# Optimization experiments

Hardware: AMD Instinct MI355X
Metric: run time of the kernel (lower is better)

Reference implementation:

```python
import jax, jax.numpy as jnp
import numpy as np

# FPN level layout for a 1024x1024 input image
LEVEL_HW = [(128, 128), (64, 64), (32, 32), (16, 16), (8, 8)]
STRIDES = [8, 16, 32, 64, 128]
IMG = 1024.0
NUM_CLASSES = 80
SCORE_THRESH = 0.2
NMS_THRESH = 0.6
TOPK = 1000
DETS = 100
BATCH = 8
TOTAL = sum(h * w for h, w in LEVEL_HW)  # 21824


def _make_anchors():
    rows = []
    for (h, w), s in zip(LEVEL_HW, STRIDES):
        xs = (np.arange(w, dtype=np.float32) + 0.5) * s
        ys = (np.arange(h, dtype=np.float32) + 0.5) * s
        xx, yy = np.meshgrid(xs, ys, indexing='ij')  # x-major, matches transpose(2,3) flatten
        pts = np.stack([xx.ravel(), yy.ravel(), xx.ravel(), yy.ravel()], axis=1)
        rows.append(pts)
    return np.concatenate(rows, axis=0).astype(np.float32)


def setup_inputs() -> dict:
    key = jax.random.key(0)
    k1, k2, k3 = jax.random.split(key, 3)
    cls_logits = jax.random.normal(k1, (BATCH, TOTAL, NUM_CLASSES), dtype=jnp.float32)
    bbox_regression = jax.random.uniform(k2, (BATCH, TOTAL, 4), dtype=jnp.float32) * 64.0
    bbox_ctrness = jax.random.normal(k3, (BATCH, TOTAL, 1), dtype=jnp.float32)
    anchors = jnp.asarray(_make_anchors())
    return {"cls_logits": cls_logits, "bbox_regression": bbox_regression,
            "bbox_ctrness": bbox_ctrness, "anchors": anchors}


def _iou_matrix(b):
    # b: [N,4] -> [N,N] pairwise IoU
    area = jnp.clip(b[:, 2] - b[:, 0], 0) * jnp.clip(b[:, 3] - b[:, 1], 0)
    lt = jnp.maximum(b[:, None, :2], b[None, :, :2])
    rb = jnp.minimum(b[:, None, 2:], b[None, :, 2:])
    wh = jnp.clip(rb - lt, 0)
    inter = wh[..., 0] * wh[..., 1]
    union = area[:, None] + area[None, :] - inter
    return inter / jnp.maximum(union, 1e-9)


def _postprocess_one(logits, reg, ctr, anchors):
    boxes_l, scores_l, labels_l = [], [], []
    off = 0
    for (h, w) in LEVEL_HW:
        n = h * w
        lg = logits[off:off + n]          # [n, C]
        rg = reg[off:off + n]             # [n, 4]
        ct = ctr[off:off + n, 0]          # [n]
        an = anchors[off:off + n]         # [n, 4]
        vals = lg.max(axis=-1)
        cls = jnp.argmax(lg, axis=-1)
        sc = jnp.sqrt(jax.nn.sigmoid(vals) * jax.nn.sigmoid(ct))
        # masked threshold + top-k  ==  filter-then-topk of the original
        masked = jnp.where(sc > SCORE_THRESH, sc, -1.0)
        k = min(TOPK, n)
        tv, ti = jax.lax.top_k(masked, k)
        a = an[ti]
        r = rg[ti]
        cx = (a[:, 0] + a[:, 2]) * 0.5
        cy = (a[:, 1] + a[:, 3]) * 0.5
        bx = jnp.stack([cx - r[:, 0], cy - r[:, 1], cx + r[:, 2], cy + r[:, 3]], axis=-1)
        bx = jnp.clip(bx, 0.0, IMG)       # clip_boxes_to_image
        boxes_l.append(bx)
        scores_l.append(tv)
        labels_l.append(cls[ti])
        off += n
    boxes = jnp.concatenate(boxes_l, axis=0)    # [N,4], N=3320
    scores = jnp.concatenate(scores_l, axis=0)  # [N]
    labels = jnp.concatenate(labels_l, axis=0)  # [N]
    N = boxes.shape[0]
    valid = scores > SCORE_THRESH
    order = jnp.argsort(-scores)
    boxes = boxes[order]
    scores = scores[order]
    labels = labels[order]
    valid = valid[order]
    # batched_nms: offset boxes per class so cross-class IoU is 0
    boff = boxes + (labels.astype(boxes.dtype) * (IMG + 1.0))[:, None]
    iou = _iou_matrix(boff)
    idx = jnp.arange(N)
    def body(i, active):
        sup = (iou[i] > NMS_THRESH) & (idx > i) & active[i]
        return active & ~sup
    active = jax.lax.fori_loop(0, N, body, valid)
    fsc = jnp.where(active, scores, -jnp.inf)
    tv, ti = jax.lax.top_k(fsc, DETS)
    m = tv > SCORE_THRESH
    out_boxes = jnp.where(m[:, None], boxes[ti], 0.0)
    out_scores = jnp.where(m, tv, 0.0)
    out_labels = jnp.where(m, labels[ti], -1)
    return out_boxes, out_scores, out_labels


def reference(cls_logits, bbox_regression, bbox_ctrness, anchors):
    fn = lambda l, r, c: _postprocess_one(l, r, c, anchors)
    boxes, scores, labels = jax.vmap(fn)(cls_logits, bbox_regression, bbox_ctrness)
    return boxes, scores, labels
```

## Files before the change

### kernel.cpp

```cpp
#include <hip/hip_runtime.h>
#include <stdint.h>

typedef unsigned long long u64;
typedef unsigned int u32;

#define BATCH   8
#define TOTAL   21824
#define NCLS    80
#define NDET    100
#define IMGSZ   1024.0f
#define STHR    0.2f
#define NMST    0.6f
#define NBUCK   2048
#define BMAX    2015
#define KGLOB   1000
#define NLOC    22

__device__ __forceinline__ float sigm(float x) { return 1.0f / (1.0f + expf(-x)); }

__device__ __forceinline__ u32 mapKm(float s) {
    u32 u = __float_as_uint(s);
    u32 m = u ^ ((u & 0x80000000u) ? 0xFFFFFFFFu : 0x80000000u);
    return ~m;
}
__device__ __forceinline__ u64 makeKey(float s, u32 idx) {
    return (((u64)mapKm(s)) << 32) | (u64)idx;
}

__device__ __forceinline__ int bucketOfV(float s) {
    int b = (int)(__fmul_rn(__fsub_rn(1.0f, s), 2520.0f));
    return b > BMAX ? BMAX : b;
}

__device__ __forceinline__ bool suppress(float4 a, float4 c) {
    float aa = __fmul_rn(fmaxf(__fsub_rn(a.z, a.x), 0.f), fmaxf(__fsub_rn(a.w, a.y), 0.f));
    float ac = __fmul_rn(fmaxf(__fsub_rn(c.z, c.x), 0.f), fmaxf(__fsub_rn(c.w, c.y), 0.f));
    float ltx = fmaxf(a.x, c.x), lty = fmaxf(a.y, c.y);
    float rbx = fminf(a.z, c.z), rby = fminf(a.w, c.w);
    float iw = fmaxf(__fsub_rn(rbx, ltx), 0.f), ih = fmaxf(__fsub_rn(rby, lty), 0.f);
    float inter = __fmul_rn(iw, ih);
    float uni = __fsub_rn(__fadd_rn(aa, ac), inter);
    float iou = __fdiv_rn(inter, fmaxf(uni, 1e-9f));
    return iou > NMST;
}

__global__ __launch_bounds__(256) void score_kernel(
        const float* __restrict__ logits, const float* __restrict__ ctr,
        float* __restrict__ mscore, int* __restrict__ mlabel) {
    const int b = blockIdx.y;
    const int tid = threadIdx.x;
    const int wave = tid >> 6, lane = tid & 63;
    const int g = lane >> 2, j = lane & 3;
    const int rowBase = blockIdx.x * 256 + wave * 64;
#pragma unroll
    for (int t = 0; t < 4; t++) {
        int r = rowBase + 16 * t + g;
        bool valid = r < TOTAL;
        float best = -1e30f; int bi = 0;
        if (valid) {
            const float* rowp = logits + ((size_t)b * TOTAL + r) * NCLS + j * 4;
#pragma unroll
            for (int u = 0; u < 5; u++) {
                float4 v = *(const float4*)(rowp + u * 16);
                int c0 = u * 16 + j * 4;
                if (v.x > best) { best = v.x; bi = c0; }
                if (v.y > best) { best = v.y; bi = c0 + 1; }
                if (v.z > best) { best = v.z; bi = c0 + 2; }
                if (v.w > best) { best = v.w; bi = c0 + 3; }
            }
        }
#pragma unroll
        for (int off = 1; off <= 2; off <<= 1) {
            float ob = __shfl_xor(best, off);
            int obi = __shfl_xor(bi, off);
            if (ob > best || (ob == best && obi < bi)) { best = ob; bi = obi; }
        }
        if (valid && j == 0) {
            float c = ctr[(size_t)b * TOTAL + r];
            float sc = sqrtf(sigm(best) * sigm(c));
            float msc = (sc > STHR) ? sc : -1.0f;
            mscore[(size_t)b * TOTAL + r] = msc;
            mlabel[(size_t)b * TOTAL + r] = bi;
        }
    }
}

__global__ __launch_bounds__(1024) void nms_kernel(
        const float* __restrict__ mscore, const int* __restrict__ mlabel,
        const float* __restrict__ anchors, const float* __restrict__ reg,
        float* __restrict__ out) {
    __shared__ u32 hist[NBUCK];
    __shared__ u64 skey[2048];
    __shared__ u32 waveSum[16], waveOff[16];
    __shared__ u32 sh_B, sh_m;
    __shared__ int s_count;
    __shared__ int accI[NDET];
    __shared__ float4 accB[NDET];
    __shared__ float4 accR[NDET];
    __shared__ int wIdx[64];
    __shared__ float4 wb[64], wraw[64];
    __shared__ u64 wsup[64];
    __shared__ u32 s_rej32[2];

    const int b = blockIdx.x, tid = threadIdx.x;
    const int wave = tid >> 6, lane = tid & 63;
    const float* ms = mscore + (size_t)b * TOTAL;

    hist[tid] = 0; hist[tid + 1024] = 0;
    if (tid == 0) { s_count = 0; sh_B = (u32)BMAX; }
    __syncthreads();

    float sv[NLOC];
    {
        int nl = 0;
        for (int i = tid; i < TOTAL; i += 1024) {
            float s0 = ms[i];
            sv[nl++] = s0;
            if (s0 > STHR) atomicAdd(&hist[bucketOfV(s0)], 1u);
        }
    }
    __syncthreads();

    u32 h0 = hist[2 * tid], h1 = hist[2 * tid + 1];
    u32 s = h0 + h1;
    u32 incl = s;
    for (int o = 1; o < 64; o <<= 1) {
        u32 t2 = (u32)__shfl_up((int)incl, o);
        if (lane >= o) incl += t2;
    }
    if (lane == 63) waveSum[wave] = incl;
    __syncthreads();
    if (tid == 0) {
        u32 acc = 0;
#pragma unroll
        for (int w = 0; w < 16; w++) { waveOff[w] = acc; acc += waveSum[w]; }
        sh_m = acc;
    }
    __syncthreads();
    const u32 E = waveOff[wave] + incl - s;
    if (E < KGLOB && KGLOB <= E + h0)            { sh_B = (u32)(2 * tid);     sh_m = E + h0; }
    else if (E + h0 < KGLOB && KGLOB <= E + h0 + h1) { sh_B = (u32)(2 * tid + 1); sh_m = E + h0 + h1; }
    hist[2 * tid] = E;
    hist[2 * tid + 1] = E + h0;
    __syncthreads();
    const int Bstar = (int)sh_B;

    {
        int nl = 0;
        for (int i = tid; i < TOTAL; i += 1024) {
            float s0 = sv[nl++];
            if (s0 > STHR) {
                int bk = bucketOfV(s0);
                if (bk <= Bstar) {
                    int pos = (int)atomicAdd(&hist[bk], 1u);
                    if (pos < 2048) skey[pos] = makeKey(s0, (u32)i);
                }
            }
        }
    }
    __syncthreads();

#pragma unroll
    for (int q = 0; q < 2; q++) {
        int bk = 2 * tid + q;
        u32 cnt = q ? h1 : h0;
        if (bk <= Bstar && cnt > 1) {
            int lo = (int)(q ? (E + h0) : E);
            int hi = lo + (int)cnt; if (hi > 2048) hi = 2048;
            for (int i2 = lo + 1; i2 < hi; i2++) {
                u64 key = skey[i2];
                int j2 = i2 - 1;
                while (j2 >= lo && skey[j2] > key) { skey[j2 + 1] = skey[j2]; j2--; }
                skey[j2 + 1] = key;
            }
        }
    }
    __syncthreads();
    int m = (int)sh_m; if (m > 2048) m = 2048;

    int count = 0, Ew = 0;
    while (true) {
        int take = m - Ew; if (take > 64) take = 64;
        if (take <= 0) break;

        if (tid < take) {
            int idx = (int)(skey[Ew + tid] & 0xFFFFFFFFu);
            float4 a = ((const float4*)anchors)[idx];
            float4 r = ((const float4*)reg)[(size_t)b * TOTAL + idx];
            float cx = (a.x + a.z) * 0.5f;
            float cy = (a.y + a.w) * 0.5f;
            float x1 = fminf(fmaxf(cx - r.x, 0.0f), IMGSZ);
            float y1 = fminf(fmaxf(cy - r.y, 0.0f), IMGSZ);
            float x2 = fminf(fmaxf(cx + r.z, 0.0f), IMGSZ);
            float y2 = fminf(fmaxf(cy + r.w, 0.0f), IMGSZ);
            float4 raw = make_float4(x1, y1, x2, y2);
            float off = (float)mlabel[(size_t)b * TOTAL + idx] * (IMGSZ + 1.0f);
            float4 ob = make_float4(__fadd_rn(x1, off), __fadd_rn(y1, off),
                                    __fadd_rn(x2, off), __fadd_rn(y2, off));
            wraw[tid] = raw; wb[tid] = ob; wIdx[tid] = idx;
        }
        if (tid < 2) s_rej32[tid] = 0;
        __syncthreads();

        {
            bool rej = false;
            if (lane < take) {
                for (int s2 = wave; s2 < count; s2 += 16) {
                    if (suppress(accB[s2], wb[lane])) { rej = true; break; }
                }
            }
            u64 mask = __ballot(rej);
            if (lane == 0 && mask) {
                u32 lo = (u32)mask, hi = (u32)(mask >> 32);
                if (lo) atomicOr(&s_rej32[0], lo);
                if (hi) atomicOr(&s_rej32[1], hi);
            }
        }
        for (int rr = wave; rr < take; rr += 16) {
            bool sp = false;
            if (lane < take && lane > rr) sp = suppress(wb[rr], wb[lane]);
            u64 mask = __ballot(sp);
            if (lane == 0) wsup[rr] = mask;
        }
        __syncthreads();

        if (wave == 0) {
            u64 supr = (lane < take) ? wsup[lane] : 0;
            u64 rejM = (u64)s_rej32[0] | ((u64)s_rej32[1] << 32);
            u64 aliveM = ((take >= 64) ? ~0ull : ((1ull << take) - 1ull)) & ~rejM;
            u64 accM = 0;
            for (int rr = 0; rr < take; rr++) {
                if ((aliveM >> rr) & 1) {
                    accM |= 1ull << rr;
                    u64 sr = __shfl(supr, rr);
                    aliveM &= ~sr;
                }
            }
            int na = __popcll(accM);
            int space = NDET - count;
            int takeA = na < space ? na : space;
            if (lane < take && ((accM >> lane) & 1)) {
                int pos = __popcll(accM & ((1ull << lane) - 1ull));
                if (pos < takeA) {
                    accI[count + pos] = wIdx[lane];
                    accB[count + pos] = wb[lane];
                    accR[count + pos] = wraw[lane];
                }
            }
            if (lane == 0) s_count = count + takeA;
        }
        __syncthreads();
        count = s_count;
        Ew += take;
        if (count >= NDET) break;
    }
    __syncthreads();

    for (int s2 = tid; s2 < NDET; s2 += 1024) {
        float4 bxv = make_float4(0.f, 0.f, 0.f, 0.f);
        float scv = 0.0f, lbv = -1.0f;
        if (s2 < count) {
            int idx = accI[s2];
            bxv = accR[s2];
            scv = ms[idx];
            lbv = (float)mlabel[(size_t)b * TOTAL + idx];
        }
        ((float4*)out)[b * NDET + s2] = bxv;
        out[BATCH * NDET * 4 + b * NDET + s2] = scv;
        out[BATCH * NDET * 4 + BATCH * NDET + b * NDET + s2] = lbv;
    }
}

extern "C" void kernel_launch(void* const* d_in, const int* in_sizes, int n_in,
                              void* d_out, int out_size, void* d_ws, size_t ws_size,
                              hipStream_t stream) {
    (void)in_sizes; (void)n_in; (void)out_size; (void)ws_size;
    const float* logits  = (const float*)d_in[0];
    const float* reg     = (const float*)d_in[1];
    const float* ctr     = (const float*)d_in[2];
    const float* anchors = (const float*)d_in[3];
    float* out = (float*)d_out;

    char* ws = (char*)d_ws;
    size_t off = 0;
    auto alloc = [&](size_t bytes) -> void* {
        off = (off + 255) & ~(size_t)255;
        void* p = ws + off;
        off += bytes;
        return p;
    };
    float* mscore = (float*)alloc((size_t)BATCH * TOTAL * 4);
    int*   mlabel = (int*)  alloc((size_t)BATCH * TOTAL * 4);

    score_kernel<<<dim3((TOTAL + 255) / 256, BATCH), 256, 0, stream>>>(logits, ctr, mscore, mlabel);
    nms_kernel<<<BATCH, 1024, 0, stream>>>(mscore, mlabel, anchors, reg, out);
}
```

Baseline: 145.0 us.

## Build score histogram in score kernel via global atomics instead of NMS kernel

```diff
diff --git a/kernel.cpp b/kernel.cpp
--- a/kernel.cpp
+++ b/kernel.cpp
@@ -44,9 +44,14 @@
     return iou > NMST;
 }
 
+__global__ __launch_bounds__(256) void zero_hist(u32* __restrict__ g) {
+    ((uint4*)g)[blockIdx.x * 256 + threadIdx.x] = make_uint4(0u, 0u, 0u, 0u);
+}
+
 __global__ __launch_bounds__(256) void score_kernel(
         const float* __restrict__ logits, const float* __restrict__ ctr,
-        float* __restrict__ mscore, int* __restrict__ mlabel) {
+        float* __restrict__ mscore, int* __restrict__ mlabel,
+        u32* __restrict__ ghist) {
     const int b = blockIdx.y;
     const int tid = threadIdx.x;
     const int wave = tid >> 6, lane = tid & 63;
@@ -78,9 +83,10 @@
         if (valid && j == 0) {
             float c = ctr[(size_t)b * TOTAL + r];
             float sc = sqrtf(sigm(best) * sigm(c));
-            float msc = (sc > STHR) ? sc : -1.0f;
-            mscore[(size_t)b * TOTAL + r] = msc;
+            bool pass = sc > STHR;
+            mscore[(size_t)b * TOTAL + r] = pass ? sc : -1.0f;
             mlabel[(size_t)b * TOTAL + r] = bi;
+            if (pass) atomicAdd(&ghist[(size_t)b * NBUCK + bucketOfV(sc)], 1u);
         }
     }
 }
@@ -88,8 +94,8 @@
 __global__ __launch_bounds__(1024) void nms_kernel(
         const float* __restrict__ mscore, const int* __restrict__ mlabel,
         const float* __restrict__ anchors, const float* __restrict__ reg,
-        float* __restrict__ out) {
-    __shared__ u32 hist[NBUCK];
+        const u32* __restrict__ ghist, float* __restrict__ out) {
+    __shared__ u32 cur[NBUCK];
     __shared__ u64 skey[2048];
     __shared__ u32 waveSum[16], waveOff[16];
     __shared__ u32 sh_B, sh_m;
@@ -106,22 +112,16 @@
     const int wave = tid >> 6, lane = tid & 63;
     const float* ms = mscore + (size_t)b * TOTAL;
 
-    hist[tid] = 0; hist[tid + 1024] = 0;
-    if (tid == 0) { s_count = 0; sh_B = (u32)BMAX; }
-    __syncthreads();
+    uint2 hv = ((const uint2*)(ghist + (size_t)b * NBUCK))[tid];
 
     float sv[NLOC];
-    {
-        int nl = 0;
-        for (int i = tid; i < TOTAL; i += 1024) {
-            float s0 = ms[i];
-            sv[nl++] = s0;
-            if (s0 > STHR) atomicAdd(&hist[bucketOfV(s0)], 1u);
-        }
-    }
-    __syncthreads();
-
-    u32 h0 = hist[2 * tid], h1 = hist[2 * tid + 1];
+#pragma unroll
+    for (int k = 0; k < NLOC; k++) {
+        int i = tid + (k << 10);
+        sv[k] = (i < TOTAL) ? ms[i] : -1.0f;
+    }
+
+    u32 h0 = hv.x, h1 = hv.y;
     u32 s = h0 + h1;
     u32 incl = s;
     for (int o = 1; o < 64; o <<= 1) {
@@ -135,26 +135,26 @@
 #pragma unroll
         for (int w = 0; w < 16; w++) { waveOff[w] = acc; acc += waveSum[w]; }
         sh_m = acc;
+        sh_B = (u32)BMAX;
+        s_count = 0;
     }
     __syncthreads();
     const u32 E = waveOff[wave] + incl - s;
     if (E < KGLOB && KGLOB <= E + h0)            { sh_B = (u32)(2 * tid);     sh_m = E + h0; }
     else if (E + h0 < KGLOB && KGLOB <= E + h0 + h1) { sh_B = (u32)(2 * tid + 1); sh_m = E + h0 + h1; }
-    hist[2 * tid] = E;
-    hist[2 * tid + 1] = E + h0;
+    cur[2 * tid] = E;
+    cur[2 * tid + 1] = E + h0;
     __syncthreads();
     const int Bstar = (int)sh_B;
 
-    {
-        int nl = 0;
-        for (int i = tid; i < TOTAL; i += 1024) {
-            float s0 = sv[nl++];
-            if (s0 > STHR) {
-                int bk = bucketOfV(s0);
-                if (bk <= Bstar) {
-                    int pos = (int)atomicAdd(&hist[bk], 1u);
-                    if (pos < 2048) skey[pos] = makeKey(s0, (u32)i);
-                }
+#pragma unroll
+    for (int k = 0; k < NLOC; k++) {
+        float s0 = sv[k];
+        if (s0 > STHR) {
+            int bk = bucketOfV(s0);
+            if (bk <= Bstar) {
+                int pos = (int)atomicAdd(&cur[bk], 1u);
+                if (pos < 2048) skey[pos] = makeKey(s0, (u32)(tid + (k << 10)));
             }
         }
     }
@@ -291,7 +291,9 @@
     };
     float* mscore = (float*)alloc((size_t)BATCH * TOTAL * 4);
     int*   mlabel = (int*)  alloc((size_t)BATCH * TOTAL * 4);
-
-    score_kernel<<<dim3((TOTAL + 255) / 256, BATCH), 256, 0, stream>>>(logits, ctr, mscore, mlabel);
-    nms_kernel<<<BATCH, 1024, 0, stream>>>(mscore, mlabel, anchors, reg, out);
-}
+    u32*   ghist  = (u32*)  alloc((size_t)BATCH * NBUCK * 4);
+
+    zero_hist<<<dim3((BATCH * NBUCK) / (256 * 4)), 256, 0, stream>>>(ghist);
+    score_kernel<<<dim3((TOTAL + 255) / 256, BATCH), 256, 0, stream>>>(logits, ctr, mscore, mlabel, ghist);
+    nms_kernel<<<BATCH, 1024, 0, stream>>>(mscore, mlabel, anchors, reg, ghist, out);
+}
```

Measured after the change: 143.3 us. About the same (-1.2%).
